# Performance work log

Measured on AMD Instinct MI355X. Metric: run time of the kernel, lower is better.

Reference implementation:

```python
import jax, jax.numpy as jnp
import numpy as np

N = 50000      # nodes
E = 800000     # edges (before self-loops)
IN = 128       # in_channels
HID = 64       # hidden_channels
HEADS = 2
OUT = 64       # out_channels (final layer, heads=1, concat=False)
NEG_SLOPE = 0.2
SM_EPS = 1e-16
BN_EPS = 1e-5


def _gat_layer(h, src, dst, W, a_src, a_dst, b, heads, outc, concat):
    """PyG GATConv (eval mode, self-loops already in src/dst)."""
    n = h.shape[0]
    g = (h @ W).reshape(n, heads, outc)                 # [N,H,C]
    al_s = jnp.sum(g * a_src, axis=-1)                  # [N,H]
    al_d = jnp.sum(g * a_dst, axis=-1)                  # [N,H]
    e = al_s[src] + al_d[dst]                           # [E,H]
    e = jnp.where(e > 0, e, NEG_SLOPE * e)              # LeakyReLU
    m = jax.ops.segment_max(e, dst, num_segments=n)     # segment softmax (stable)
    ee = jnp.exp(e - m[dst])
    s = jax.ops.segment_sum(ee, dst, num_segments=n)
    alpha = ee / (s[dst] + SM_EPS)                      # [E,H]
    out = jax.ops.segment_sum(g[src] * alpha[:, :, None], dst, num_segments=n)  # [N,H,C]
    out = out.reshape(n, heads * outc) if concat else out.mean(axis=1)
    return out + b


def _bn_eval(x, gamma, beta, mean, var):
    return (x - mean) * jax.lax.rsqrt(var + BN_EPS) * gamma + beta


def setup_inputs() -> dict:
    key = jax.random.key(0)
    ks = jax.random.split(key, 32)
    d = {}
    d["x"] = jax.random.normal(ks[0], (N, IN), jnp.float32)
    d["edge_index"] = jax.random.randint(ks[1], (2, E), 0, N, dtype=jnp.int32)
    # layer 0: IN -> HID x HEADS (concat)
    d["W0"] = jax.random.normal(ks[2], (IN, HEADS * HID), jnp.float32) * 0.05
    d["a_src0"] = jax.random.normal(ks[3], (HEADS, HID), jnp.float32) * 0.05
    d["a_dst0"] = jax.random.normal(ks[4], (HEADS, HID), jnp.float32) * 0.05
    d["b0"] = jnp.zeros((HEADS * HID,), jnp.float32)
    d["g0"] = jax.random.uniform(ks[5], (HEADS * HID,), jnp.float32, 0.5, 1.5)
    d["beta0"] = jax.random.normal(ks[6], (HEADS * HID,), jnp.float32) * 0.1
    d["m0"] = jax.random.normal(ks[7], (HEADS * HID,), jnp.float32) * 0.1
    d["v0"] = jax.random.uniform(ks[8], (HEADS * HID,), jnp.float32, 0.5, 1.5)
    # layer 1: HID*HEADS -> HID x HEADS (concat)
    d["W1"] = jax.random.normal(ks[9], (HEADS * HID, HEADS * HID), jnp.float32) * 0.05
    d["a_src1"] = jax.random.normal(ks[10], (HEADS, HID), jnp.float32) * 0.05
    d["a_dst1"] = jax.random.normal(ks[11], (HEADS, HID), jnp.float32) * 0.05
    d["b1"] = jnp.zeros((HEADS * HID,), jnp.float32)
    d["g1"] = jax.random.uniform(ks[12], (HEADS * HID,), jnp.float32, 0.5, 1.5)
    d["beta1"] = jax.random.normal(ks[13], (HEADS * HID,), jnp.float32) * 0.1
    d["m1"] = jax.random.normal(ks[14], (HEADS * HID,), jnp.float32) * 0.1
    d["v1"] = jax.random.uniform(ks[15], (HEADS * HID,), jnp.float32, 0.5, 1.5)
    # layer 2: HID*HEADS -> OUT, heads=1, concat=False
    d["W2"] = jax.random.normal(ks[16], (HEADS * HID, OUT), jnp.float32) * 0.05
    d["a_src2"] = jax.random.normal(ks[17], (1, OUT), jnp.float32) * 0.05
    d["a_dst2"] = jax.random.normal(ks[18], (1, OUT), jnp.float32) * 0.05
    d["b2"] = jnp.zeros((OUT,), jnp.float32)
    return d


def reference(x, edge_index, W0, a_src0, a_dst0, b0, g0, beta0, m0, v0,
              W1, a_src1, a_dst1, b1, g1, beta1, m1, v1,
              W2, a_src2, a_dst2, b2):
    n = x.shape[0]
    loops = jnp.arange(n, dtype=edge_index.dtype)
    src = jnp.concatenate([edge_index[0], loops])   # PyG add_self_loops=True
    dst = jnp.concatenate([edge_index[1], loops])
    h = _gat_layer(x, src, dst, W0, a_src0, a_dst0, b0, HEADS, HID, True)
    h = jax.nn.relu(_bn_eval(h, g0, beta0, m0, v0))   # eval: dropout inactive
    h = _gat_layer(h, src, dst, W1, a_src1, a_dst1, b1, HEADS, HID, True)
    h = jax.nn.relu(_bn_eval(h, g1, beta1, m1, v1))
    out = _gat_layer(h, src, dst, W2, a_src2, a_dst2, b2, 1, OUT, False)
    return out
```

## Files before the change

### kernel.cpp

```cpp
#include <hip/hip_runtime.h>
#include <hip/hip_fp16.h>
#include <cstdint>

#define NEG_SLOPE 0.2f
#define SM_EPS 1e-16f
#define BN_EPS 1e-5f

struct alignas(8)  half4v { __half2 lo, hi; };
struct alignas(16) half8v { __half2 h0, h1, h2, h3; };

__device__ __forceinline__ void fma8(float* acc, const half8v& g, float w) {
  float2 f0 = __half22float2(g.h0), f1 = __half22float2(g.h1);
  float2 f2 = __half22float2(g.h2), f3 = __half22float2(g.h3);
  acc[0] = fmaf(w, f0.x, acc[0]); acc[1] = fmaf(w, f0.y, acc[1]);
  acc[2] = fmaf(w, f1.x, acc[2]); acc[3] = fmaf(w, f1.y, acc[3]);
  acc[4] = fmaf(w, f2.x, acc[4]); acc[5] = fmaf(w, f2.y, acc[5]);
  acc[6] = fmaf(w, f3.x, acc[6]); acc[7] = fmaf(w, f3.y, acc[7]);
}

template <int INC, int OUTC, int H>
__global__ __launch_bounds__(256) void gemm_k(const float* __restrict__ A,
                                              const float* __restrict__ W,
                                              const float* __restrict__ asrc,
                                              const float* __restrict__ adst,
                                              __half* __restrict__ G,
                                              float* __restrict__ als,
                                              float* __restrict__ ald, int nrows) {
  constexpr int TPR  = OUTC / 4;
  constexpr int RS   = 256 / TPR;
  constexpr int ROWS = RS * 4;
  __shared__ float wl[INC * OUTC];
  __shared__ float hl[ROWS * INC];
  for (int i = threadIdx.x * 4; i < INC * OUTC; i += 1024)
    *(float4*)&wl[i] = *(const float4*)&W[i];
  int r  = threadIdx.x / TPR;
  int c0 = (threadIdx.x % TPR) * 4;
  float4 sv = *(const float4*)&asrc[c0];
  float4 dv = *(const float4*)&adst[c0];
  for (int base = blockIdx.x * ROWS; base < nrows; base += gridDim.x * ROWS) {
    __syncthreads();
    int limit = min(ROWS, nrows - base) * INC;
    for (int i = threadIdx.x * 4; i < limit; i += 1024)
      *(float4*)&hl[i] = *(const float4*)&A[(size_t)base * INC + i];
    __syncthreads();
    float acc[4][4];
#pragma unroll
    for (int q = 0; q < 4; q++)
#pragma unroll
      for (int c = 0; c < 4; c++) acc[q][c] = 0.f;
#pragma unroll 8
    for (int k = 0; k < INC; k++) {
      float4 wv = *(float4*)&wl[k * OUTC + c0];
#pragma unroll
      for (int q = 0; q < 4; q++) {
        float h = hl[(r + q * RS) * INC + k];
        acc[q][0] = fmaf(h, wv.x, acc[q][0]);
        acc[q][1] = fmaf(h, wv.y, acc[q][1]);
        acc[q][2] = fmaf(h, wv.z, acc[q][2]);
        acc[q][3] = fmaf(h, wv.w, acc[q][3]);
      }
    }
    float ps[4], pd[4];
#pragma unroll
    for (int q = 0; q < 4; q++) {
      int rq = base + r + q * RS;
      if (rq < nrows) {
        half4v hv;
        hv.lo = __floats2half2_rn(acc[q][0], acc[q][1]);
        hv.hi = __floats2half2_rn(acc[q][2], acc[q][3]);
        *(half4v*)&G[(size_t)rq * OUTC + c0] = hv;
      }
      ps[q] = acc[q][0] * sv.x + acc[q][1] * sv.y + acc[q][2] * sv.z + acc[q][3] * sv.w;
      pd[q] = acc[q][0] * dv.x + acc[q][1] * dv.y + acc[q][2] * dv.z + acc[q][3] * dv.w;
    }
#pragma unroll
    for (int o = 1; o < 16; o <<= 1) {
#pragma unroll
      for (int q = 0; q < 4; q++) {
        ps[q] += __shfl_xor(ps[q], o);
        pd[q] += __shfl_xor(pd[q], o);
      }
    }
    if ((threadIdx.x & 15) == 0) {
      int head = c0 >> 6;
#pragma unroll
      for (int q = 0; q < 4; q++) {
        int rq = base + r + q * RS;
        if (rq < nrows) {
          als[(size_t)rq * H + head] = ps[q];
          ald[(size_t)rq * H + head] = pd[q];
        }
      }
    }
  }
}

__global__ __launch_bounds__(256) void deg_k(const int* __restrict__ dst, int E_,
                                             int n, int* __restrict__ deg) {
  int g   = blockIdx.x & 7;
  int npg = (n + 7) / 8;
  int n0  = g * npg;
  int n1  = min(n0 + npg, n);
  int bg  = blockIdx.x >> 3;
  int nbg = gridDim.x >> 3;
  int ET  = E_ + n;
  for (int e = bg * 256 + threadIdx.x; e < ET; e += nbg * 256) {
    int dN = (e < E_) ? dst[e] : (e - E_);
    if (dN >= n0 && dN < n1) atomicAdd(&deg[dN], 1);
  }
}

__global__ __launch_bounds__(1024) void scan1_k(const int* __restrict__ deg,
                                                int* __restrict__ incl,
                                                int* __restrict__ bsum, int n) {
  __shared__ int sm[1024];
  int i = blockIdx.x * 1024 + threadIdx.x;
  int v = (i < n) ? deg[i] : 0;
  sm[threadIdx.x] = v;
  __syncthreads();
#pragma unroll
  for (int o = 1; o < 1024; o <<= 1) {
    int t = (threadIdx.x >= o) ? sm[threadIdx.x - o] : 0;
    __syncthreads();
    sm[threadIdx.x] += t;
    __syncthreads();
  }
  if (i < n) incl[i] = sm[threadIdx.x];
  if (threadIdx.x == 1023) bsum[blockIdx.x] = sm[1023];
}

__global__ void scan2_k(int* __restrict__ bsum, int nb) {
  int lane = threadIdx.x;
  int v = (lane < nb) ? bsum[lane] : 0;
#pragma unroll
  for (int o = 1; o < 64; o <<= 1) {
    int t = __shfl_up(v, o);
    if (lane >= o) v += t;
  }
  if (lane < nb) bsum[lane] = v;
}

__global__ void scan3_k(const int* __restrict__ incl, const int* __restrict__ bsum,
                        const int* __restrict__ deg, int* __restrict__ rowptr,
                        int* __restrict__ cursor, int n) {
  int i = blockIdx.x * blockDim.x + threadIdx.x;
  if (i < n) {
    int blk = i >> 10;
    int off = blk ? bsum[blk - 1] : 0;
    int r = incl[i] + off;
    rowptr[i + 1] = r;
    cursor[i] = r - deg[i];
  }
  if (i == 0) rowptr[0] = 0;
}

__global__ __launch_bounds__(256) void csr_fill_k(const int* __restrict__ src,
                                                  const int* __restrict__ dst, int E_,
                                                  int n, int* __restrict__ cursor,
                                                  uint16_t* __restrict__ csr_src) {
  int g   = blockIdx.x & 7;
  int npg = (n + 7) / 8;
  int n0  = g * npg;
  int n1  = min(n0 + npg, n);
  int bg  = blockIdx.x >> 3;
  int nbg = gridDim.x >> 3;
  int ET  = E_ + n;
  for (int e = bg * 256 + threadIdx.x; e < ET; e += nbg * 256) {
    int dN = (e < E_) ? dst[e] : (e - E_);
    if (dN >= n0 && dN < n1) {
      int sN  = (e < E_) ? src[e] : dN;
      int pos = atomicAdd(&cursor[dN], 1);
      csr_src[pos] = (uint16_t)sN;
    }
  }
}

__global__ __launch_bounds__(256) void csr_canon_k(const int* __restrict__ rowptr,
                                                   uint16_t* __restrict__ csr, int n) {
  int l   = threadIdx.x & 31;
  int grp = (blockIdx.x * blockDim.x + threadIdx.x) >> 5;
  int ng  = (gridDim.x * blockDim.x) >> 5;
  for (int node = grp; node < n; node += ng) {
    int beg = rowptr[node];
    int deg = rowptr[node + 1] - beg;
    if (deg <= 1) continue;
    if (deg <= 128) {
      int iters = (deg + 31) >> 5;
      uint16_t v[4];
      int      rk[4];
#pragma unroll
      for (int m = 0; m < 4; m++) {
        if (m >= iters) break;
        int  i   = l + m * 32;
        bool act = i < deg;
        uint16_t vi = act ? csr[beg + i] : (uint16_t)0;
        int rank = 0;
        for (int j = 0; j < deg; j++) {
          uint16_t vj = csr[beg + j];
          rank += (int)((vj < vi) | ((vj == vi) & (j < i)));
        }
        v[m]  = vi;
        rk[m] = act ? rank : -1;
      }
#pragma unroll
      for (int m = 0; m < 4; m++) {
        if (m >= iters) break;
        if (rk[m] >= 0) csr[beg + rk[m]] = v[m];
      }
    } else if (l == 0) {
      for (int i = beg + 1; i < beg + deg; ++i) {
        uint16_t vv = csr[i];
        int j = i - 1;
        while (j >= beg && csr[j] > vv) { csr[j + 1] = csr[j]; --j; }
        csr[j + 1] = vv;
      }
    }
  }
}

__global__ __launch_bounds__(256) void gat_agg2_k(
    const int* __restrict__ rowptr, const uint16_t* __restrict__ csr_src,
    const float* __restrict__ als, const float* __restrict__ ald,
    const __half* __restrict__ G, const float* __restrict__ bias,
    const float* __restrict__ gamma, const float* __restrict__ beta,
    const float* __restrict__ mean, const float* __restrict__ var,
    float* __restrict__ out, int n) {
  int l   = threadIdx.x & 31;
  int grp = (blockIdx.x * blockDim.x + threadIdx.x) >> 5;
  int ng  = (gridDim.x * blockDim.x) >> 5;
  int ehi = l >> 4;
  int sub = l & 15;
  int cc  = sub * 8;
  bool hh = sub >= 8;
  for (int node = grp; node < n; node += ng) {
    int beg = rowptr[node];
    int deg = rowptr[node + 1] - beg;
    float2 adp = *(const float2*)&ald[(size_t)node * 2];
    float accP[8], accQ[8];
#pragma unroll
    for (int k = 0; k < 8; k++) { accP[k] = 0.f; accQ[k] = 0.f; }
    if (deg <= 32) {
      int sl_ = 0;
      float p0 = 0.f, p1 = 0.f;
      if (l < deg) {
        sl_ = csr_src[beg + l];
        float2 ap = *(const float2*)&als[(size_t)sl_ * 2];
        float v0 = ap.x + adp.x, v1 = ap.y + adp.y;
        v0 = v0 > 0.f ? v0 : NEG_SLOPE * v0;
        v1 = v1 > 0.f ? v1 : NEG_SLOPE * v1;
        p0 = __expf(v0); p1 = __expf(v1);
      }
      float s0 = p0, s1 = p1;
#pragma unroll
      for (int o = 1; o < 32; o <<= 1) {
        s0 += __shfl_xor(s0, o, 32);
        s1 += __shfl_xor(s1, o, 32);
      }
      float a0 = p0 / (s0 + SM_EPS);
      float a1 = p1 / (s1 + SM_EPS);
      for (int i = 0; i < deg; i += 8) {
        int e0 = i + ehi, e1 = i + 2 + ehi, e2 = i + 4 + ehi, e3 = i + 6 + ehi;
        int sA = __shfl(sl_, e0, 32);
        int sB = __shfl(sl_, e1, 32);
        int sC = __shfl(sl_, e2, 32);
        int sD = __shfl(sl_, e3, 32);
        float wA0 = __shfl(a0, e0, 32), wA1 = __shfl(a1, e0, 32);
        float wB0 = __shfl(a0, e1, 32), wB1 = __shfl(a1, e1, 32);
        float wC0 = __shfl(a0, e2, 32), wC1 = __shfl(a1, e2, 32);
        float wD0 = __shfl(a0, e3, 32), wD1 = __shfl(a1, e3, 32);
        float wA = hh ? wA1 : wA0, wB = hh ? wB1 : wB0;
        float wC = hh ? wC1 : wC0, wD = hh ? wD1 : wD0;
        half8v gA = *(const half8v*)&G[(size_t)sA * 128 + cc];
        half8v gB = *(const half8v*)&G[(size_t)sB * 128 + cc];
        half8v gC = *(const half8v*)&G[(size_t)sC * 128 + cc];
        half8v gD = *(const half8v*)&G[(size_t)sD * 128 + cc];
        fma8(accP, gA, wA);
        fma8(accQ, gB, wB);
        fma8(accP, gC, wC);
        fma8(accQ, gD, wD);
      }
    } else {
      float s0 = 0.f, s1 = 0.f;
      for (int i = l; i < deg; i += 32) {
        int s = csr_src[beg + i];
        float2 ap = *(const float2*)&als[(size_t)s * 2];
        float v0 = ap.x + adp.x; v0 = v0 > 0.f ? v0 : NEG_SLOPE * v0;
        float v1 = ap.y + adp.y; v1 = v1 > 0.f ? v1 : NEG_SLOPE * v1;
        s0 += __expf(v0); s1 += __expf(v1);
      }
#pragma unroll
      for (int o = 1; o < 32; o <<= 1) {
        s0 += __shfl_xor(s0, o, 32);
        s1 += __shfl_xor(s1, o, 32);
      }
      float inv0 = 1.f / (s0 + SM_EPS);
      float inv1 = 1.f / (s1 + SM_EPS);
      for (int i = 0; i < deg; i += 2) {
        int  e   = i + ehi;
        bool act = e < deg;
        int  sE  = 0;
        float w  = 0.f;
        if (act) {
          sE = csr_src[beg + e];
          float2 ap = *(const float2*)&als[(size_t)sE * 2];
          float v0 = ap.x + adp.x; v0 = v0 > 0.f ? v0 : NEG_SLOPE * v0;
          float v1 = ap.y + adp.y; v1 = v1 > 0.f ? v1 : NEG_SLOPE * v1;
          w = hh ? (__expf(v1) * inv1) : (__expf(v0) * inv0);
        }
        half8v g = *(const half8v*)&G[(size_t)sE * 128 + cc];
        fma8(accP, g, w);
      }
    }
    float o8[8];
#pragma unroll
    for (int k = 0; k < 8; k++) {
      o8[k] = accP[k] + accQ[k];
      o8[k] += __shfl_xor(o8[k], 16, 32);
    }
    if (l < 16) {
      float4 bv0 = *(const float4*)&bias[cc],  bv1 = *(const float4*)&bias[cc + 4];
      float4 mv0 = *(const float4*)&mean[cc],  mv1 = *(const float4*)&mean[cc + 4];
      float4 vv0 = *(const float4*)&var[cc],   vv1 = *(const float4*)&var[cc + 4];
      float4 gv0 = *(const float4*)&gamma[cc], gv1 = *(const float4*)&gamma[cc + 4];
      float4 tv0 = *(const float4*)&beta[cc],  tv1 = *(const float4*)&beta[cc + 4];
      float4 u0, u1;
      u0.x = fmaxf((o8[0] + bv0.x - mv0.x) * rsqrtf(vv0.x + BN_EPS) * gv0.x + tv0.x, 0.f);
      u0.y = fmaxf((o8[1] + bv0.y - mv0.y) * rsqrtf(vv0.y + BN_EPS) * gv0.y + tv0.y, 0.f);
      u0.z = fmaxf((o8[2] + bv0.z - mv0.z) * rsqrtf(vv0.z + BN_EPS) * gv0.z + tv0.z, 0.f);
      u0.w = fmaxf((o8[3] + bv0.w - mv0.w) * rsqrtf(vv0.w + BN_EPS) * gv0.w + tv0.w, 0.f);
      u1.x = fmaxf((o8[4] + bv1.x - mv1.x) * rsqrtf(vv1.x + BN_EPS) * gv1.x + tv1.x, 0.f);
      u1.y = fmaxf((o8[5] + bv1.y - mv1.y) * rsqrtf(vv1.y + BN_EPS) * gv1.y + tv1.y, 0.f);
      u1.z = fmaxf((o8[6] + bv1.z - mv1.z) * rsqrtf(vv1.z + BN_EPS) * gv1.z + tv1.z, 0.f);
      u1.w = fmaxf((o8[7] + bv1.w - mv1.w) * rsqrtf(vv1.w + BN_EPS) * gv1.w + tv1.w, 0.f);
      *(float4*)&out[(size_t)node * 128 + cc]     = u0;
      *(float4*)&out[(size_t)node * 128 + cc + 4] = u1;
    }
  }
}

__global__ __launch_bounds__(256) void gat_agg1_k(
    const int* __restrict__ rowptr, const uint16_t* __restrict__ csr_src,
    const float* __restrict__ als, const float* __restrict__ ald,
    const __half* __restrict__ G, const float* __restrict__ bias,
    float* __restrict__ out, int n) {
  int l   = threadIdx.x & 31;
  int grp = (blockIdx.x * blockDim.x + threadIdx.x) >> 5;
  int ng  = (gridDim.x * blockDim.x) >> 5;
  int e8  = l >> 3;
  int sub = l & 7;
  int cc  = sub * 8;
  for (int node = grp; node < n; node += ng) {
    int beg = rowptr[node];
    int deg = rowptr[node + 1] - beg;
    float ad0 = ald[node];
    float accP[8], accQ[8];
#pragma unroll
    for (int k = 0; k < 8; k++) { accP[k] = 0.f; accQ[k] = 0.f; }
    if (deg <= 32) {
      int sl_ = 0;
      float p0 = 0.f;
      if (l < deg) {
        sl_ = csr_src[beg + l];
        float v0 = als[sl_] + ad0;
        v0 = v0 > 0.f ? v0 : NEG_SLOPE * v0;
        p0 = __expf(v0);
      }
      float s0 = p0;
#pragma unroll
      for (int o = 1; o < 32; o <<= 1) s0 += __shfl_xor(s0, o, 32);
      float a0 = p0 / (s0 + SM_EPS);
      for (int i = 0; i < deg; i += 16) {
        int e0 = i + e8, e1 = i + 4 + e8, e2 = i + 8 + e8, e3 = i + 12 + e8;
        int sA = __shfl(sl_, e0, 32);
        int sB = __shfl(sl_, e1, 32);
        int sC = __shfl(sl_, e2, 32);
        int sD = __shfl(sl_, e3, 32);
        float wA = __shfl(a0, e0, 32);
        float wB = __shfl(a0, e1, 32);
        float wC = __shfl(a0, e2, 32);
        float wD = __shfl(a0, e3, 32);
        half8v gA = *(const half8v*)&G[(size_t)sA * 64 + cc];
        half8v gB = *(const half8v*)&G[(size_t)sB * 64 + cc];
        half8v gC = *(const half8v*)&G[(size_t)sC * 64 + cc];
        half8v gD = *(const half8v*)&G[(size_t)sD * 64 + cc];
        fma8(accP, gA, wA);
        fma8(accQ, gB, wB);
        fma8(accP, gC, wC);
        fma8(accQ, gD, wD);
      }
    } else {
      float s0 = 0.f;
      for (int i = l; i < deg; i += 32) {
        int s = csr_src[beg + i];
        float v0 = als[s] + ad0; v0 = v0 > 0.f ? v0 : NEG_SLOPE * v0;
        s0 += __expf(v0);
      }
#pragma unroll
      for (int o = 1; o < 32; o <<= 1) s0 += __shfl_xor(s0, o, 32);
      float inv0 = 1.f / (s0 + SM_EPS);
      for (int i = 0; i < deg; i += 4) {
        int  e   = i + e8;
        bool act = e < deg;
        int  sE  = 0;
        float w  = 0.f;
        if (act) {
          sE = csr_src[beg + e];
          float v0 = als[sE] + ad0; v0 = v0 > 0.f ? v0 : NEG_SLOPE * v0;
          w = __expf(v0) * inv0;
        }
        half8v g = *(const half8v*)&G[(size_t)sE * 64 + cc];
        fma8(accP, g, w);
      }
    }
    float o8[8];
#pragma unroll
    for (int k = 0; k < 8; k++) {
      o8[k] = accP[k] + accQ[k];
      o8[k] += __shfl_xor(o8[k], 8, 32);
      o8[k] += __shfl_xor(o8[k], 16, 32);
    }
    if (l < 8) {
      float4 bv0 = *(const float4*)&bias[cc], bv1 = *(const float4*)&bias[cc + 4];
      float4 u0 = make_float4(o8[0] + bv0.x, o8[1] + bv0.y, o8[2] + bv0.z, o8[3] + bv0.w);
      float4 u1 = make_float4(o8[4] + bv1.x, o8[5] + bv1.y, o8[6] + bv1.z, o8[7] + bv1.w);
      *(float4*)&out[(size_t)node * 64 + cc]     = u0;
      *(float4*)&out[(size_t)node * 64 + cc + 4] = u1;
    }
  }
}

extern "C" void kernel_launch(void* const* d_in, const int* in_sizes, int n_in,
                              void* d_out, int out_size, void* d_ws, size_t ws_size,
                              hipStream_t stream) {
  const float* x   = (const float*)d_in[0];
  const int*   ei  = (const int*)d_in[1];
  const float* W0  = (const float*)d_in[2];
  const float* as0 = (const float*)d_in[3];
  const float* ad0 = (const float*)d_in[4];
  const float* b0  = (const float*)d_in[5];
  const float* gm0 = (const float*)d_in[6];
  const float* bt0 = (const float*)d_in[7];
  const float* mu0 = (const float*)d_in[8];
  const float* vr0 = (const float*)d_in[9];
  const float* W1  = (const float*)d_in[10];
  const float* as1 = (const float*)d_in[11];
  const float* ad1 = (const float*)d_in[12];
  const float* b1  = (const float*)d_in[13];
  const float* gm1 = (const float*)d_in[14];
  const float* bt1 = (const float*)d_in[15];
  const float* mu1 = (const float*)d_in[16];
  const float* vr1 = (const float*)d_in[17];
  const float* W2  = (const float*)d_in[18];
  const float* as2 = (const float*)d_in[19];
  const float* ad2 = (const float*)d_in[20];
  const float* b2  = (const float*)d_in[21];

  int N  = in_sizes[0] / 128;
  int E  = in_sizes[1] / 2;
  int ET = E + N;
  const int* srcp = ei;
  const int* dstp = ei + E;

  char* w = (char*)d_ws;
  auto carve = [&](size_t bytes) {
    void* p = (void*)w;
    w += (bytes + 255) & ~(size_t)255;
    return p;
  };
  __half*   G      = (__half*)carve((size_t)N * 128 * 2);
  float*    Hb     = (float*)carve((size_t)N * 128 * 4);
  float*    ALS    = (float*)carve((size_t)N * 2 * 4);
  float*    ALD    = (float*)carve((size_t)N * 2 * 4);
  int*      DEG    = (int*)carve((size_t)N * 4);
  int*      INCL   = (int*)carve((size_t)N * 4);
  int*      BSUM   = (int*)carve((size_t)64 * 4);
  int*      ROWPTR = (int*)carve((size_t)(N + 1) * 4);
  int*      CURSOR = (int*)carve((size_t)N * 4);
  uint16_t* CSRSRC = (uint16_t*)carve((size_t)ET * 2);

  int agrid = (N + 7) / 8;
  int nblk  = (N + 1023) / 1024;

  hipMemsetAsync(DEG, 0, (size_t)N * 4, stream);
  deg_k<<<2048, 256, 0, stream>>>(dstp, E, N, DEG);
  scan1_k<<<nblk, 1024, 0, stream>>>(DEG, INCL, BSUM, N);
  scan2_k<<<1, 64, 0, stream>>>(BSUM, nblk);
  scan3_k<<<(N + 255) / 256, 256, 0, stream>>>(INCL, BSUM, DEG, ROWPTR, CURSOR, N);
  csr_fill_k<<<2048, 256, 0, stream>>>(srcp, dstp, E, N, CURSOR, CSRSRC);
  csr_canon_k<<<agrid, 256, 0, stream>>>(ROWPTR, CSRSRC, N);

  gemm_k<128, 128, 2><<<512, 256, 0, stream>>>(x, W0, as0, ad0, G, ALS, ALD, N);
  gat_agg2_k<<<agrid, 256, 0, stream>>>(ROWPTR, CSRSRC, ALS, ALD, G, b0, gm0, bt0,
                                        mu0, vr0, Hb, N);
  gemm_k<128, 128, 2><<<512, 256, 0, stream>>>(Hb, W1, as1, ad1, G, ALS, ALD, N);
  gat_agg2_k<<<agrid, 256, 0, stream>>>(ROWPTR, CSRSRC, ALS, ALD, G, b1, gm1, bt1,
                                        mu1, vr1, Hb, N);
  gemm_k<128, 64, 1><<<512, 256, 0, stream>>>(Hb, W2, as2, ad2, G, ALS, ALD, N);
  gat_agg1_k<<<agrid, 256, 0, stream>>>(ROWPTR, CSRSRC, ALS, ALD, G, b2,
                                        (float*)d_out, N);
}
```

Measured before the change: 311.4 us.

## Process four nodes per 32-lane group with batched softmax prologue in aggregation kernels

Each 32-lane group in the GAT aggregation kernels now handles four consecutive destination nodes instead of grid-striding one node at a time. Row pointers, degrees, dst attention terms and source indices for all four nodes are loaded up front, and their softmax weights are computed before any feature gathering starts. The goal is to expose more independent memory loads so the latency of the dependent rowptr, csr and als chain is hidden. The aggregation grid shrinks by four, which reduces parallelism, and register pressure rises.

```diff
diff --git a/kernel.cpp b/kernel.cpp
--- a/kernel.cpp
+++ b/kernel.cpp
@@ -227,37 +227,61 @@
     float* __restrict__ out, int n) {
   int l   = threadIdx.x & 31;
   int grp = (blockIdx.x * blockDim.x + threadIdx.x) >> 5;
-  int ng  = (gridDim.x * blockDim.x) >> 5;
   int ehi = l >> 4;
   int sub = l & 15;
   int cc  = sub * 8;
   bool hh = sub >= 8;
-  for (int node = grp; node < n; node += ng) {
-    int beg = rowptr[node];
-    int deg = rowptr[node + 1] - beg;
-    float2 adp = *(const float2*)&ald[(size_t)node * 2];
+  int node0 = grp * 4;
+  if (node0 >= n) return;
+
+  int   begq[4], degq[4], slq[4];
+  float a0q[4], a1q[4];
+  float adx[4], ady[4];
+#pragma unroll
+  for (int q = 0; q < 4; q++) {
+    int nd = node0 + q;
+    begq[q] = 0; degq[q] = 0; slq[q] = 0; a0q[q] = 0.f; a1q[q] = 0.f;
+    adx[q] = 0.f; ady[q] = 0.f;
+    if (nd < n) {
+      begq[q] = rowptr[nd];
+      degq[q] = rowptr[nd + 1] - begq[q];
+      float2 adp = *(const float2*)&ald[(size_t)nd * 2];
+      adx[q] = adp.x; ady[q] = adp.y;
+      if (degq[q] <= 32 && l < degq[q]) slq[q] = csr_src[begq[q] + l];
+    }
+  }
+#pragma unroll
+  for (int q = 0; q < 4; q++) {
+    if (node0 + q >= n || degq[q] > 32) continue;
+    float p0 = 0.f, p1 = 0.f;
+    if (l < degq[q]) {
+      float2 ap = *(const float2*)&als[(size_t)slq[q] * 2];
+      float v0 = ap.x + adx[q], v1 = ap.y + ady[q];
+      v0 = v0 > 0.f ? v0 : NEG_SLOPE * v0;
+      v1 = v1 > 0.f ? v1 : NEG_SLOPE * v1;
+      p0 = __expf(v0); p1 = __expf(v1);
+    }
+    float s0 = p0, s1 = p1;
+#pragma unroll
+    for (int o = 1; o < 32; o <<= 1) {
+      s0 += __shfl_xor(s0, o, 32);
+      s1 += __shfl_xor(s1, o, 32);
+    }
+    a0q[q] = p0 / (s0 + SM_EPS);
+    a1q[q] = p1 / (s1 + SM_EPS);
+  }
+
+#pragma unroll
+  for (int q = 0; q < 4; q++) {
+    int nd = node0 + q;
+    if (nd >= n) continue;
+    int   beg = begq[q], deg = degq[q];
     float accP[8], accQ[8];
 #pragma unroll
     for (int k = 0; k < 8; k++) { accP[k] = 0.f; accQ[k] = 0.f; }
     if (deg <= 32) {
-      int sl_ = 0;
-      float p0 = 0.f, p1 = 0.f;
-      if (l < deg) {
-        sl_ = csr_src[beg + l];
-        float2 ap = *(const float2*)&als[(size_t)sl_ * 2];
-        float v0 = ap.x + adp.x, v1 = ap.y + adp.y;
-        v0 = v0 > 0.f ? v0 : NEG_SLOPE * v0;
-        v1 = v1 > 0.f ? v1 : NEG_SLOPE * v1;
-        p0 = __expf(v0); p1 = __expf(v1);
-      }
-      float s0 = p0, s1 = p1;
-#pragma unroll
-      for (int o = 1; o < 32; o <<= 1) {
-        s0 += __shfl_xor(s0, o, 32);
-        s1 += __shfl_xor(s1, o, 32);
-      }
-      float a0 = p0 / (s0 + SM_EPS);
-      float a1 = p1 / (s1 + SM_EPS);
+      int   sl_ = slq[q];
+      float a0 = a0q[q], a1 = a1q[q];
       for (int i = 0; i < deg; i += 8) {
         int e0 = i + ehi, e1 = i + 2 + ehi, e2 = i + 4 + ehi, e3 = i + 6 + ehi;
         int sA = __shfl(sl_, e0, 32);
@@ -280,12 +304,13 @@
         fma8(accQ, gD, wD);
       }
     } else {
+      float adpx = adx[q], adpy = ady[q];
       float s0 = 0.f, s1 = 0.f;
       for (int i = l; i < deg; i += 32) {
         int s = csr_src[beg + i];
         float2 ap = *(const float2*)&als[(size_t)s * 2];
-        float v0 = ap.x + adp.x; v0 = v0 > 0.f ? v0 : NEG_SLOPE * v0;
-        float v1 = ap.y + adp.y; v1 = v1 > 0.f ? v1 : NEG_SLOPE * v1;
+        float v0 = ap.x + adpx; v0 = v0 > 0.f ? v0 : NEG_SLOPE * v0;
+        float v1 = ap.y + adpy; v1 = v1 > 0.f ? v1 : NEG_SLOPE * v1;
         s0 += __expf(v0); s1 += __expf(v1);
       }
 #pragma unroll
@@ -303,8 +328,8 @@
         if (act) {
           sE = csr_src[beg + e];
           float2 ap = *(const float2*)&als[(size_t)sE * 2];
-          float v0 = ap.x + adp.x; v0 = v0 > 0.f ? v0 : NEG_SLOPE * v0;
-          float v1 = ap.y + adp.y; v1 = v1 > 0.f ? v1 : NEG_SLOPE * v1;
+          float v0 = ap.x + adpx; v0 = v0 > 0.f ? v0 : NEG_SLOPE * v0;
+          float v1 = ap.y + adpy; v1 = v1 > 0.f ? v1 : NEG_SLOPE * v1;
           w = hh ? (__expf(v1) * inv1) : (__expf(v0) * inv0);
         }
         half8v g = *(const half8v*)&G[(size_t)sE * 128 + cc];
@@ -332,8 +357,8 @@
       u1.y = fmaxf((o8[5] + bv1.y - mv1.y) * rsqrtf(vv1.y + BN_EPS) * gv1.y + tv1.y, 0.f);
       u1.z = fmaxf((o8[6] + bv1.z - mv1.z) * rsqrtf(vv1.z + BN_EPS) * gv1.z + tv1.z, 0.f);
       u1.w = fmaxf((o8[7] + bv1.w - mv1.w) * rsqrtf(vv1.w + BN_EPS) * gv1.w + tv1.w, 0.f);
-      *(float4*)&out[(size_t)node * 128 + cc]     = u0;
-      *(float4*)&out[(size_t)node * 128 + cc + 4] = u1;
+      *(float4*)&out[(size_t)nd * 128 + cc]     = u0;
+      *(float4*)&out[(size_t)nd * 128 + cc + 4] = u1;
     }
   }
 }
@@ -345,30 +370,51 @@
     float* __restrict__ out, int n) {
   int l   = threadIdx.x & 31;
   int grp = (blockIdx.x * blockDim.x + threadIdx.x) >> 5;
-  int ng  = (gridDim.x * blockDim.x) >> 5;
   int e8  = l >> 3;
   int sub = l & 7;
   int cc  = sub * 8;
-  for (int node = grp; node < n; node += ng) {
-    int beg = rowptr[node];
-    int deg = rowptr[node + 1] - beg;
-    float ad0 = ald[node];
+  int node0 = grp * 4;
+  if (node0 >= n) return;
+
+  int   begq[4], degq[4], slq[4];
+  float a0q[4], adq[4];
+#pragma unroll
+  for (int q = 0; q < 4; q++) {
+    int nd = node0 + q;
+    begq[q] = 0; degq[q] = 0; slq[q] = 0; a0q[q] = 0.f; adq[q] = 0.f;
+    if (nd < n) {
+      begq[q] = rowptr[nd];
+      degq[q] = rowptr[nd + 1] - begq[q];
+      adq[q]  = ald[nd];
+      if (degq[q] <= 32 && l < degq[q]) slq[q] = csr_src[begq[q] + l];
+    }
+  }
+#pragma unroll
+  for (int q = 0; q < 4; q++) {
+    if (node0 + q >= n || degq[q] > 32) continue;
+    float p0 = 0.f;
+    if (l < degq[q]) {
+      float v0 = als[slq[q]] + adq[q];
+      v0 = v0 > 0.f ? v0 : NEG_SLOPE * v0;
+      p0 = __expf(v0);
+    }
+    float s0 = p0;
+#pragma unroll
+    for (int o = 1; o < 32; o <<= 1) s0 += __shfl_xor(s0, o, 32);
+    a0q[q] = p0 / (s0 + SM_EPS);
+  }
+
+#pragma unroll
+  for (int q = 0; q < 4; q++) {
+    int nd = node0 + q;
+    if (nd >= n) continue;
+    int beg = begq[q], deg = degq[q];
     float accP[8], accQ[8];
 #pragma unroll
     for (int k = 0; k < 8; k++) { accP[k] = 0.f; accQ[k] = 0.f; }
     if (deg <= 32) {
-      int sl_ = 0;
-      float p0 = 0.f;
-      if (l < deg) {
-        sl_ = csr_src[beg + l];
-        float v0 = als[sl_] + ad0;
-        v0 = v0 > 0.f ? v0 : NEG_SLOPE * v0;
-        p0 = __expf(v0);
-      }
-      float s0 = p0;
-#pragma unroll
-      for (int o = 1; o < 32; o <<= 1) s0 += __shfl_xor(s0, o, 32);
-      float a0 = p0 / (s0 + SM_EPS);
+      int   sl_ = slq[q];
+      float a0  = a0q[q];
       for (int i = 0; i < deg; i += 16) {
         int e0 = i + e8, e1 = i + 4 + e8, e2 = i + 8 + e8, e3 = i + 12 + e8;
         int sA = __shfl(sl_, e0, 32);
@@ -389,6 +435,7 @@
         fma8(accQ, gD, wD);
       }
     } else {
+      float ad0 = adq[q];
       float s0 = 0.f;
       for (int i = l; i < deg; i += 32) {
         int s = csr_src[beg + i];
@@ -423,8 +470,8 @@
       float4 bv0 = *(const float4*)&bias[cc], bv1 = *(const float4*)&bias[cc + 4];
       float4 u0 = make_float4(o8[0] + bv0.x, o8[1] + bv0.y, o8[2] + bv0.z, o8[3] + bv0.w);
       float4 u1 = make_float4(o8[4] + bv1.x, o8[5] + bv1.y, o8[6] + bv1.z, o8[7] + bv1.w);
-      *(float4*)&out[(size_t)node * 64 + cc]     = u0;
-      *(float4*)&out[(size_t)node * 64 + cc + 4] = u1;
+      *(float4*)&out[(size_t)nd * 64 + cc]     = u0;
+      *(float4*)&out[(size_t)nd * 64 + cc + 4] = u1;
     }
   }
 }
@@ -478,7 +525,8 @@
   int*      CURSOR = (int*)carve((size_t)N * 4);
   uint16_t* CSRSRC = (uint16_t*)carve((size_t)ET * 2);
 
-  int agrid = (N + 7) / 8;
+  int cgrid = (N + 7) / 8;
+  int agrid = (N + 31) / 32;
   int nblk  = (N + 1023) / 1024;
 
   hipMemsetAsync(DEG, 0, (size_t)N * 4, stream);
@@ -487,7 +535,7 @@
   scan2_k<<<1, 64, 0, stream>>>(BSUM, nblk);
   scan3_k<<<(N + 255) / 256, 256, 0, stream>>>(INCL, BSUM, DEG, ROWPTR, CURSOR, N);
   csr_fill_k<<<2048, 256, 0, stream>>>(srcp, dstp, E, N, CURSOR, CSRSRC);
-  csr_canon_k<<<agrid, 256, 0, stream>>>(ROWPTR, CSRSRC, N);
+  csr_canon_k<<<cgrid, 256, 0, stream>>>(ROWPTR, CSRSRC, N);
 
   gemm_k<128, 128, 2><<<512, 256, 0, stream>>>(x, W0, as0, ad0, G, ALS, ALD, N);
   gat_agg2_k<<<agrid, 256, 0, stream>>>(ROWPTR, CSRSRC, ALS, ALD, G, b0, gm0, bt0,
```

New measurement: 330.6 us. 6.2% more time.

## Replace FP32 LDS-tiled GEMM with fp16 MFMA GEMM using prepacked weights

Applied to the files above, without the earlier changes.

Swaps the scalar FMA shared-memory GEMM for a wave-level MFMA 16x16x32 fp16 kernel. Activations are converted to fp16 in registers and weights are pre-packed once per call into MFMA fragment layout by a new pack kernel. The attention-logit dot products are computed from the MFMA accumulators with a shuffle reduction. The aim is to cut the dense transform cost, at the price of fp16 rounding of inputs and weights and uncoalesced scalar half stores of G.

```diff
diff --git a/kernel.cpp b/kernel.cpp
--- a/kernel.cpp
+++ b/kernel.cpp
@@ -8,6 +8,9 @@
 
 struct alignas(8)  half4v { __half2 lo, hi; };
 struct alignas(16) half8v { __half2 h0, h1, h2, h3; };
+
+typedef _Float16 f16x8 __attribute__((ext_vector_type(8)));
+typedef float    f32x4 __attribute__((ext_vector_type(4)));
 
 __device__ __forceinline__ void fma8(float* acc, const half8v& g, float w) {
   float2 f0 = __half22float2(g.h0), f1 = __half22float2(g.h1);
@@ -18,77 +21,100 @@
   acc[6] = fmaf(w, f3.x, acc[6]); acc[7] = fmaf(w, f3.y, acc[7]);
 }
 
-template <int INC, int OUTC, int H>
-__global__ __launch_bounds__(256) void gemm_k(const float* __restrict__ A,
-                                              const float* __restrict__ W,
-                                              const float* __restrict__ asrc,
-                                              const float* __restrict__ adst,
-                                              __half* __restrict__ G,
-                                              float* __restrict__ als,
-                                              float* __restrict__ ald, int nrows) {
-  constexpr int TPR  = OUTC / 4;
-  constexpr int RS   = 256 / TPR;
-  constexpr int ROWS = RS * 4;
-  __shared__ float wl[INC * OUTC];
-  __shared__ float hl[ROWS * INC];
-  for (int i = threadIdx.x * 4; i < INC * OUTC; i += 1024)
-    *(float4*)&wl[i] = *(const float4*)&W[i];
-  int r  = threadIdx.x / TPR;
-  int c0 = (threadIdx.x % TPR) * 4;
-  float4 sv = *(const float4*)&asrc[c0];
-  float4 dv = *(const float4*)&adst[c0];
-  for (int base = blockIdx.x * ROWS; base < nrows; base += gridDim.x * ROWS) {
-    __syncthreads();
-    int limit = min(ROWS, nrows - base) * INC;
-    for (int i = threadIdx.x * 4; i < limit; i += 1024)
-      *(float4*)&hl[i] = *(const float4*)&A[(size_t)base * INC + i];
-    __syncthreads();
-    float acc[4][4];
-#pragma unroll
-    for (int q = 0; q < 4; q++)
-#pragma unroll
-      for (int c = 0; c < 4; c++) acc[q][c] = 0.f;
-#pragma unroll 8
-    for (int k = 0; k < INC; k++) {
-      float4 wv = *(float4*)&wl[k * OUTC + c0];
-#pragma unroll
-      for (int q = 0; q < 4; q++) {
-        float h = hl[(r + q * RS) * INC + k];
-        acc[q][0] = fmaf(h, wv.x, acc[q][0]);
-        acc[q][1] = fmaf(h, wv.y, acc[q][1]);
-        acc[q][2] = fmaf(h, wv.z, acc[q][2]);
-        acc[q][3] = fmaf(h, wv.w, acc[q][3]);
-      }
-    }
-    float ps[4], pd[4];
-#pragma unroll
-    for (int q = 0; q < 4; q++) {
-      int rq = base + r + q * RS;
-      if (rq < nrows) {
-        half4v hv;
-        hv.lo = __floats2half2_rn(acc[q][0], acc[q][1]);
-        hv.hi = __floats2half2_rn(acc[q][2], acc[q][3]);
-        *(half4v*)&G[(size_t)rq * OUTC + c0] = hv;
-      }
-      ps[q] = acc[q][0] * sv.x + acc[q][1] * sv.y + acc[q][2] * sv.z + acc[q][3] * sv.w;
-      pd[q] = acc[q][0] * dv.x + acc[q][1] * dv.y + acc[q][2] * dv.z + acc[q][3] * dv.w;
+__global__ void packW_k(const float* __restrict__ W0, const float* __restrict__ W1,
+                        const float* __restrict__ W2, _Float16* __restrict__ P0,
+                        _Float16* __restrict__ P1, _Float16* __restrict__ P2) {
+  int t = blockIdx.x * 256 + threadIdx.x;
+  const float* W; _Float16* P; int OUTC, idx;
+  if (t < 16384)      { W = W0; P = P0; OUTC = 128; idx = t; }
+  else if (t < 32768) { W = W1; P = P1; OUTC = 128; idx = t - 16384; }
+  else if (t < 40960) { W = W2; P = P2; OUTC = 64;  idx = t - 32768; }
+  else return;
+  int j = idx & 7, lane = (idx >> 3) & 63, kt = (idx >> 9) & 3, ct = idx >> 11;
+  int k = kt * 32 + (lane >> 4) * 8 + j;
+  int c = ct * 16 + (lane & 15);
+  P[idx] = (_Float16)W[k * OUTC + c];
+}
+
+template <int OUTC, int H>
+__global__ __launch_bounds__(256) void gemm_mfma_k(
+    const float* __restrict__ A, const _Float16* __restrict__ Wp,
+    const float* __restrict__ asrc, const float* __restrict__ adst,
+    __half* __restrict__ G, float* __restrict__ als, float* __restrict__ ald,
+    int nrows) {
+  constexpr int CT = OUTC / 16;
+  int wid = threadIdx.x >> 6;
+  int l   = threadIdx.x & 63;
+  int r16 = l & 15;
+  int kb  = l >> 4;
+  for (int base = blockIdx.x * 64 + wid * 16; base < nrows; base += gridDim.x * 64) {
+    int arow = base + r16; if (arow >= nrows) arow = nrows - 1;
+    const float* ap = &A[(size_t)arow * 128];
+    f16x8 af[4];
+#pragma unroll
+    for (int kt = 0; kt < 4; kt++) {
+      float4 x0 = *(const float4*)&ap[kt * 32 + kb * 8];
+      float4 x1 = *(const float4*)&ap[kt * 32 + kb * 8 + 4];
+      f16x8 v;
+      v[0] = (_Float16)x0.x; v[1] = (_Float16)x0.y;
+      v[2] = (_Float16)x0.z; v[3] = (_Float16)x0.w;
+      v[4] = (_Float16)x1.x; v[5] = (_Float16)x1.y;
+      v[6] = (_Float16)x1.z; v[7] = (_Float16)x1.w;
+      af[kt] = v;
+    }
+    f32x4 acc[CT];
+#pragma unroll
+    for (int ct = 0; ct < CT; ct++) {
+      f32x4 a = {0.f, 0.f, 0.f, 0.f};
+#pragma unroll
+      for (int kt = 0; kt < 4; kt++) {
+        f16x8 bf = *(const f16x8*)&Wp[(size_t)(((ct * 4 + kt) * 64 + l)) * 8];
+        a = __builtin_amdgcn_mfma_f32_16x16x32_f16(af[kt], bf, a, 0, 0, 0);
+      }
+      acc[ct] = a;
+    }
+    float ps0[4] = {0, 0, 0, 0}, ps1[4] = {0, 0, 0, 0};
+    float pd0[4] = {0, 0, 0, 0}, pd1[4] = {0, 0, 0, 0};
+#pragma unroll
+    for (int ct = 0; ct < CT; ct++) {
+      int col = ct * 16 + r16;
+      float as_ = asrc[col], ad_ = adst[col];
+      bool h1 = (H == 2) && (col >= 64);
+#pragma unroll
+      for (int r = 0; r < 4; r++) {
+        float v = acc[ct][r];
+        int rowD = base + kb * 4 + r;
+        if (rowD < nrows) G[(size_t)rowD * OUTC + col] = __float2half(v);
+        if (h1) { ps1[r] = fmaf(v, as_, ps1[r]); pd1[r] = fmaf(v, ad_, pd1[r]); }
+        else    { ps0[r] = fmaf(v, as_, ps0[r]); pd0[r] = fmaf(v, ad_, pd0[r]); }
+      }
     }
 #pragma unroll
     for (int o = 1; o < 16; o <<= 1) {
 #pragma unroll
-      for (int q = 0; q < 4; q++) {
-        ps[q] += __shfl_xor(ps[q], o);
-        pd[q] += __shfl_xor(pd[q], o);
-      }
-    }
-    if ((threadIdx.x & 15) == 0) {
-      int head = c0 >> 6;
-#pragma unroll
-      for (int q = 0; q < 4; q++) {
-        int rq = base + r + q * RS;
-        if (rq < nrows) {
-          als[(size_t)rq * H + head] = ps[q];
-          ald[(size_t)rq * H + head] = pd[q];
+      for (int r = 0; r < 4; r++) {
+        ps0[r] += __shfl_xor(ps0[r], o);
+        pd0[r] += __shfl_xor(pd0[r], o);
+        if (H == 2) {
+          ps1[r] += __shfl_xor(ps1[r], o);
+          pd1[r] += __shfl_xor(pd1[r], o);
+        }
+      }
+    }
+    if (r16 == 0) {
+#pragma unroll
+      for (int r = 0; r < 4; r++) {
+        int rowD = base + kb * 4 + r;
+        if (rowD < nrows) {
+          if (H == 2) {
+            als[(size_t)rowD * 2]     = ps0[r];
+            als[(size_t)rowD * 2 + 1] = ps1[r];
+            ald[(size_t)rowD * 2]     = pd0[r];
+            ald[(size_t)rowD * 2 + 1] = pd1[r];
+          } else {
+            als[rowD] = ps0[r];
+            ald[rowD] = pd0[r];
+          }
         }
       }
     }
@@ -467,35 +493,41 @@
     w += (bytes + 255) & ~(size_t)255;
     return p;
   };
-  __half*   G      = (__half*)carve((size_t)N * 128 * 2);
-  float*    Hb     = (float*)carve((size_t)N * 128 * 4);
-  float*    ALS    = (float*)carve((size_t)N * 2 * 4);
-  float*    ALD    = (float*)carve((size_t)N * 2 * 4);
-  int*      DEG    = (int*)carve((size_t)N * 4);
-  int*      INCL   = (int*)carve((size_t)N * 4);
-  int*      BSUM   = (int*)carve((size_t)64 * 4);
-  int*      ROWPTR = (int*)carve((size_t)(N + 1) * 4);
-  int*      CURSOR = (int*)carve((size_t)N * 4);
-  uint16_t* CSRSRC = (uint16_t*)carve((size_t)ET * 2);
-
+  __half*    G      = (__half*)carve((size_t)N * 128 * 2);
+  float*     Hb     = (float*)carve((size_t)N * 128 * 4);
+  float*     ALS    = (float*)carve((size_t)N * 2 * 4);
+  float*     ALD    = (float*)carve((size_t)N * 2 * 4);
+  int*       DEG    = (int*)carve((size_t)N * 4);
+  int*       INCL   = (int*)carve((size_t)N * 4);
+  int*       BSUM   = (int*)carve((size_t)64 * 4);
+  int*       ROWPTR = (int*)carve((size_t)(N + 1) * 4);
+  int*       CURSOR = (int*)carve((size_t)N * 4);
+  uint16_t*  CSRSRC = (uint16_t*)carve((size_t)ET * 2);
+  _Float16*  WP0    = (_Float16*)carve(16384 * 2);
+  _Float16*  WP1    = (_Float16*)carve(16384 * 2);
+  _Float16*  WP2    = (_Float16*)carve(8192 * 2);
+
+  int cgrid = (N + 7) / 8;
   int agrid = (N + 7) / 8;
+  int ggrid = (N + 63) / 64;
   int nblk  = (N + 1023) / 1024;
 
+  packW_k<<<160, 256, 0, stream>>>(W0, W1, W2, WP0, WP1, WP2);
   hipMemsetAsync(DEG, 0, (size_t)N * 4, stream);
   deg_k<<<2048, 256, 0, stream>>>(dstp, E, N, DEG);
   scan1_k<<<nblk, 1024, 0, stream>>>(DEG, INCL, BSUM, N);
   scan2_k<<<1, 64, 0, stream>>>(BSUM, nblk);
   scan3_k<<<(N + 255) / 256, 256, 0, stream>>>(INCL, BSUM, DEG, ROWPTR, CURSOR, N);
   csr_fill_k<<<2048, 256, 0, stream>>>(srcp, dstp, E, N, CURSOR, CSRSRC);
-  csr_canon_k<<<agrid, 256, 0, stream>>>(ROWPTR, CSRSRC, N);
-
-  gemm_k<128, 128, 2><<<512, 256, 0, stream>>>(x, W0, as0, ad0, G, ALS, ALD, N);
+  csr_canon_k<<<cgrid, 256, 0, stream>>>(ROWPTR, CSRSRC, N);
+
+  gemm_mfma_k<128, 2><<<ggrid, 256, 0, stream>>>(x, WP0, as0, ad0, G, ALS, ALD, N);
   gat_agg2_k<<<agrid, 256, 0, stream>>>(ROWPTR, CSRSRC, ALS, ALD, G, b0, gm0, bt0,
                                         mu0, vr0, Hb, N);
-  gemm_k<128, 128, 2><<<512, 256, 0, stream>>>(Hb, W1, as1, ad1, G, ALS, ALD, N);
+  gemm_mfma_k<128, 2><<<ggrid, 256, 0, stream>>>(Hb, WP1, as1, ad1, G, ALS, ALD, N);
   gat_agg2_k<<<agrid, 256, 0, stream>>>(ROWPTR, CSRSRC, ALS, ALD, G, b1, gm1, bt1,
                                         mu1, vr1, Hb, N);
-  gemm_k<128, 64, 1><<<512, 256, 0, stream>>>(Hb, W2, as2, ad2, G, ALS, ALD, N);
+  gemm_mfma_k<64, 1><<<ggrid, 256, 0, stream>>>(Hb, WP2, as2, ad2, G, ALS, ALD, N);
   gat_agg1_k<<<agrid, 256, 0, stream>>>(ROWPTR, CSRSRC, ALS, ALD, G, b2,
                                         (float*)d_out, N);
 }
```

Result: faster. 264.1 us (-15.2%).
